# Performance work log

Hardware: AMD Instinct MI355X
Metric: run time of the kernel (lower is better)

The kernel has to match this reference:

```python
import jax, jax.numpy as jnp
import numpy as np

EPS = 1e-5
NUM_HEADS = 8
MASK_FILL = -50000.0


def set_norm(X, fmask):
    # Masked "set" layer-norm: mean/var over ALL valid (row, feature) entries
    # of each set jointly. fmask: [B, S, 1] float (1 = valid row).
    D = X.shape[-1]
    cnt = fmask.sum(axis=(1, 2), keepdims=True) * D
    mean = (X * fmask).sum(axis=(1, 2), keepdims=True) / cnt
    var = (((X - mean) ** 2) * fmask).sum(axis=(1, 2), keepdims=True) / cnt
    return (X - mean) / jnp.sqrt(var + EPS) * fmask


def setup_inputs() -> dict:
    key = jax.random.key(0)
    ks = jax.random.split(key, 9)
    B, S, D = 8, 1024, 512
    Q = jax.random.normal(ks[0], (B, S, D), dtype=jnp.float32)
    Q = Q.at[:, 3 * S // 4:, :].set(0.0)
    scale = 0.02
    params = {
        'Wq': jax.random.normal(ks[1], (D, D), jnp.float32) * scale,
        'bq': jnp.zeros((D,), jnp.float32),
        'Wk': jax.random.normal(ks[2], (D, D), jnp.float32) * scale,
        'bk': jnp.zeros((D,), jnp.float32),
        'Wv': jax.random.normal(ks[3], (D, D), jnp.float32) * scale,
        'bv': jnp.zeros((D,), jnp.float32),
        'Wo': jax.random.normal(ks[4], (D, D), jnp.float32) * scale,
        'bo': jnp.zeros((D,), jnp.float32),
    }
    return {'Q': Q, **params}


def reference(Q, Wq, bq, Wk, bk, Wv, bv, Wo, bo):
    B, S, D = Q.shape
    H = NUM_HEADS
    hd = D // H

    # row mask: row is valid if any feature is nonzero
    row_valid = jnp.any(Q != 0, axis=-1, keepdims=True)      # [B, S, 1] bool
    fmask = row_valid.astype(Q.dtype)                        # [B, S, 1]

    # pre-norms (self-attention: K = V = Q)
    Qn = set_norm(Q, fmask)
    Kn = Qn

    # projections, re-masked
    Qp = (Qn @ Wq + bq) * fmask
    Kp = (Kn @ Wk + bk) * fmask
    Vp = (Kn @ Wv + bv) * fmask

    def to_heads(X):  # [B, S, D] -> [B, H, S, hd]
        return X.reshape(B, S, H, hd).transpose(0, 2, 1, 3)

    q, k, v = to_heads(Qp), to_heads(Kp), to_heads(Vp)

    # attn_mask: True = masked-out pair (invalid row in Q or K)
    invalid = ~(row_valid & row_valid.transpose(0, 2, 1))    # [B, S, S]
    invalid = invalid[:, None, :, :]                         # [B, 1, S, S]

    scale = 1.0 / np.sqrt(hd).astype(np.float32)
    scores = jnp.einsum('bhqd,bhkd->bhqk', q, k) * scale
    scores = scores + jnp.where(invalid, MASK_FILL, 0.0)
    # additive fill + post-softmax multiplicative mask (nonstandard pattern)
    w = jax.nn.softmax(scores, axis=-1) * (~invalid).astype(scores.dtype)

    attn = jnp.einsum('bhqk,bhkd->bhqd', w, v)               # [B, H, S, hd]
    attn = attn.transpose(0, 2, 1, 3).reshape(B, S, D)

    attn_out = attn + Q                                      # residual with raw input
    normed = set_norm(attn_out, fmask)                       # normVO (V mask == Q mask)
    out = attn_out + jax.nn.relu(normed @ Wo + bo)           # dropout p=0 -> identity
    return out, w
```

## Files before the change

### kernel.cpp

```cpp
#include <hip/hip_runtime.h>
#include <math.h>

#define BB 8
#define SS 1024
#define DD 512
#define HH 8
#define NROWS (BB*SS)
#define EPSV 1e-5f
#define SCALE_V 0.125f

#define I_SUM1 0
#define I_SS1  8
#define I_CNT  16
#define I_MEAN1 24
#define I_INV1 32
#define I_SUM2 40
#define I_SS2  48
#define I_MEAN2 56
#define I_INV2 64
#define I_TMASK 96
#define I_KBITS 224

typedef __bf16 bf16x8 __attribute__((ext_vector_type(8)));
typedef __bf16 bf16x4 __attribute__((ext_vector_type(4)));
typedef float f32x4 __attribute__((ext_vector_type(4)));

#define MFMA16(a,b,c) __builtin_amdgcn_mfma_f32_16x16x32_bf16(a,b,c,0,0,0)

#define LDSTRIDE 40
#define ASTR 72

__global__ __launch_bounds__(128) void stats1_k(const float* __restrict__ Q,
                                                float* __restrict__ fmask,
                                                float* __restrict__ stats) {
    int row = blockIdx.x;
    int b = row >> 10;
    int t = threadIdx.x;
    float4 v = *(const float4*)(Q + ((size_t)row << 9) + (t << 2));
    float s  = v.x + v.y + v.z + v.w;
    float ss = v.x*v.x + v.y*v.y + v.z*v.z + v.w*v.w;
    int nz = (v.x != 0.f) || (v.y != 0.f) || (v.z != 0.f) || (v.w != 0.f);
    __shared__ float rs[128], rss[128];
    __shared__ int rnz[128];
    rs[t] = s; rss[t] = ss; rnz[t] = nz;
    __syncthreads();
    for (int off = 64; off > 0; off >>= 1) {
        if (t < off) { rs[t] += rs[t+off]; rss[t] += rss[t+off]; rnz[t] |= rnz[t+off]; }
        __syncthreads();
    }
    if (t == 0) {
        float f = rnz[0] ? 1.f : 0.f;
        fmask[row] = f;
        if (f != 0.f) {
            atomicAdd(&stats[I_SUM1 + b], rs[0]);
            atomicAdd(&stats[I_SS1 + b], rss[0]);
            atomicAdd(&stats[I_CNT + b], 1.f);
        }
    }
}

__global__ __launch_bounds__(128) void finalize_k(float* __restrict__ stats,
                                                  const float* __restrict__ fmask,
                                                  int osum, int oss, int ocnt,
                                                  int omean, int oinv, int dotile) {
    int t = threadIdx.x;
    if (t < BB) {
        float cntD = stats[ocnt + t] * 512.f;
        float mean = stats[osum + t] / cntD;
        float var  = stats[oss + t] / cntD - mean * mean;
        stats[omean + t] = mean;
        stats[oinv + t]  = rsqrtf(var + EPSV);
    }
    if (dotile) {
        int* ip = (int*)stats;
        const float* fr = fmask + (t << 6);
        int any = 0;
        for (int i = 0; i < 64; i += 4) {
            float4 v = *(const float4*)(fr + i);
            any |= (v.x != 0.f) | (v.y != 0.f) | (v.z != 0.f) | (v.w != 0.f);
        }
        ip[I_TMASK + t] = any;
        __syncthreads();
        if (t < BB) {
            int bits = 0;
            #pragma unroll
            for (int i = 0; i < 16; ++i)
                bits |= (ip[I_TMASK + (t << 4) + i] ? 1 : 0) << i;
            ip[I_KBITS + t] = bits;
        }
    }
}

__global__ __launch_bounds__(256) void tw_k(const float* __restrict__ Wq,
                                            const float* __restrict__ Wk,
                                            const float* __restrict__ Wv,
                                            const float* __restrict__ Wo,
                                            __bf16* __restrict__ Wt) {
    int z = blockIdx.z;
    const float* W = (z == 0) ? Wq : (z == 1) ? Wk : (z == 2) ? Wv : Wo;
    __bf16* dst = Wt + ((size_t)z << 18);
    __shared__ float tile[64][65];
    int t = threadIdx.x;
    int k0 = blockIdx.y << 6, n0 = blockIdx.x << 6;
    int r = t >> 4, c = (t & 15) << 2;
    #pragma unroll
    for (int i = 0; i < 4; ++i) {
        float4 v = *(const float4*)(W + (size_t)(k0 + r + i*16) * 512 + n0 + c);
        tile[r + i*16][c+0] = v.x; tile[r + i*16][c+1] = v.y;
        tile[r + i*16][c+2] = v.z; tile[r + i*16][c+3] = v.w;
    }
    __syncthreads();
    #pragma unroll
    for (int i = 0; i < 4; ++i) {
        int n = r + i*16;
        bf16x4 o;
        o[0] = (__bf16)tile[c+0][n]; o[1] = (__bf16)tile[c+1][n];
        o[2] = (__bf16)tile[c+2][n]; o[3] = (__bf16)tile[c+3][n];
        *(bf16x4*)(dst + (size_t)(n0 + n) * 512 + k0 + c) = o;
    }
}

__global__ __launch_bounds__(256) void projqkv_k(
    const float* __restrict__ Q, const float* __restrict__ stats,
    const float* __restrict__ fmask, const __bf16* __restrict__ Wt,
    const float* __restrict__ bq, const float* __restrict__ bk,
    const float* __restrict__ bv,
    __bf16* __restrict__ Qp, __bf16* __restrict__ Kp, __bf16* __restrict__ Vt)
{
    __shared__ __align__(16) __bf16 smem[64 * LDSTRIDE * 4];
    int t = threadIdx.x;
    int m0 = blockIdx.y << 6, n0 = blockIdx.x << 6;
    int b = m0 >> 10, s0 = m0 & 1023, h = n0 >> 6;
    int bh = (b << 3) + h;
    const int* ip = (const int*)stats;
    if (!ip[I_TMASK + (m0 >> 6)]) {
        int m = t >> 2, ch = (t & 3) << 4;
        bf16x8 z = {};
        *(bf16x8*)(Qp + ((size_t)(m0 + m) << 9) + n0 + ch)     = z;
        *(bf16x8*)(Qp + ((size_t)(m0 + m) << 9) + n0 + ch + 8) = z;
        *(bf16x8*)(Kp + ((size_t)(m0 + m) << 9) + n0 + ch)     = z;
        *(bf16x8*)(Kp + ((size_t)(m0 + m) << 9) + n0 + ch + 8) = z;
        *(bf16x8*)(Vt + ((size_t)bh << 16) + ((size_t)m << 10) + s0 + ch)     = z;
        *(bf16x8*)(Vt + ((size_t)bh << 16) + ((size_t)m << 10) + s0 + ch + 8) = z;
        return;
    }
    __bf16* As = smem;
    int srow = t >> 2, skp = (t & 3) << 3;
    int arow = m0 + srow;
    float fi   = fmask[arow] * stats[I_INV1 + b];
    float mean = stats[I_MEAN1 + b];
    int wave = t >> 6, lane = t & 63, quad = lane >> 4, l16 = lane & 15;
    int aoff  = (wave * 16 + l16) * LDSTRIDE + quad * 8;
    int boff0 = l16 * LDSTRIDE + quad * 8;
    f32x4 acc[3][4] = {};
    const float*  Arow = Q + ((size_t)arow << 9);
    const __bf16* Brow = Wt + ((size_t)(n0 + srow) << 9);
    float4 a0 = *(const float4*)(Arow + skp);
    float4 a1 = *(const float4*)(Arow + skp + 4);
    bf16x8 w0 = *(const bf16x8*)(Brow + skp);
    bf16x8 w1 = *(const bf16x8*)(Brow + (1 << 18) + skp);
    bf16x8 w2 = *(const bf16x8*)(Brow + (2 << 18) + skp);
    for (int k0 = 0; k0 < 512; k0 += 32) {
        bf16x8 av;
        av[0] = (__bf16)((a0.x - mean) * fi); av[1] = (__bf16)((a0.y - mean) * fi);
        av[2] = (__bf16)((a0.z - mean) * fi); av[3] = (__bf16)((a0.w - mean) * fi);
        av[4] = (__bf16)((a1.x - mean) * fi); av[5] = (__bf16)((a1.y - mean) * fi);
        av[6] = (__bf16)((a1.z - mean) * fi); av[7] = (__bf16)((a1.w - mean) * fi);
        *(bf16x8*)&As[srow * LDSTRIDE + skp] = av;
        *(bf16x8*)&smem[64*LDSTRIDE*1 + srow * LDSTRIDE + skp] = w0;
        *(bf16x8*)&smem[64*LDSTRIDE*2 + srow * LDSTRIDE + skp] = w1;
        *(bf16x8*)&smem[64*LDSTRIDE*3 + srow * LDSTRIDE + skp] = w2;
        __syncthreads();
        if (k0 < 480) {
            a0 = *(const float4*)(Arow + k0 + 32 + skp);
            a1 = *(const float4*)(Arow + k0 + 36 + skp);
            w0 = *(const bf16x8*)(Brow + k0 + 32 + skp);
            w1 = *(const bf16x8*)(Brow + (1 << 18) + k0 + 32 + skp);
            w2 = *(const bf16x8*)(Brow + (2 << 18) + k0 + 32 + skp);
        }
        bf16x8 af = *(const bf16x8*)&As[aoff];
        #pragma unroll
        for (int nt = 0; nt < 4; ++nt) {
            int bo = boff0 + nt * (16 * LDSTRIDE);
            acc[0][nt] = MFMA16(af, *(const bf16x8*)&smem[64*LDSTRIDE*1 + bo], acc[0][nt]);
            acc[1][nt] = MFMA16(af, *(const bf16x8*)&smem[64*LDSTRIDE*2 + bo], acc[1][nt]);
            acc[2][nt] = MFMA16(af, *(const bf16x8*)&smem[64*LDSTRIDE*3 + bo], acc[2][nt]);
        }
        __syncthreads();
    }
    float fmr[4];
    #pragma unroll
    for (int reg = 0; reg < 4; ++reg) fmr[reg] = fmask[m0 + wave*16 + quad*4 + reg];
    __bf16* Cs = smem;
    #pragma unroll
    for (int z = 0; z < 2; ++z) {
        const float* bias = z ? bk : bq;
        __bf16* C = z ? Kp : Qp;
        #pragma unroll
        for (int nt = 0; nt < 4; ++nt) {
            float bn = bias[n0 + nt * 16 + l16];
            #pragma unroll
            for (int reg = 0; reg < 4; ++reg) {
                int m = wave * 16 + quad * 4 + reg;
                Cs[m * 70 + nt * 16 + l16] = (__bf16)((acc[z][nt][reg] + bn) * fmr[reg]);
            }
        }
        __syncthreads();
        int m = t >> 2, ch = (t & 3) << 4;
        bf16x8 o0 = *(const bf16x8*)&Cs[m * 70 + ch];
        bf16x8 o1 = *(const bf16x8*)&Cs[m * 70 + ch + 8];
        *(bf16x8*)(C + ((size_t)(m0 + m) << 9) + n0 + ch)     = o0;
        *(bf16x8*)(C + ((size_t)(m0 + m) << 9) + n0 + ch + 8) = o1;
        __syncthreads();
    }
    #pragma unroll
    for (int nt = 0; nt < 4; ++nt) {
        int d = nt * 16 + l16;
        float bn = bv[n0 + d];
        #pragma unroll
        for (int reg = 0; reg < 4; ++reg) {
            int sl = wave * 16 + quad * 4 + reg;
            Cs[d * 70 + sl] = (__bf16)((acc[2][nt][reg] + bn) * fmr[reg]);
        }
    }
    __syncthreads();
    {
        int d = t >> 2, seg = (t & 3) << 4;
        bf16x8 o0 = *(const bf16x8*)&Cs[d * 70 + seg];
        bf16x8 o1 = *(const bf16x8*)&Cs[d * 70 + seg + 8];
        *(bf16x8*)(Vt + ((size_t)bh << 16) + ((size_t)d << 10) + s0 + seg)     = o0;
        *(bf16x8*)(Vt + ((size_t)bh << 16) + ((size_t)d << 10) + s0 + seg + 8) = o1;
    }
}

__global__ __launch_bounds__(256) void attn_k(
    const __bf16* __restrict__ Qp, const __bf16* __restrict__ Kp,
    const __bf16* __restrict__ Vt,
    const float* __restrict__ fmask, const float* __restrict__ Q,
    float* __restrict__ stats, float* __restrict__ w, float* __restrict__ attn)
{
    int bh = blockIdx.y, b = bh >> 3, h = bh & 7;
    int q0 = blockIdx.x << 6;
    int t = threadIdx.x;
    const int* ip = (const int*)stats;
    int kb = ip[I_KBITS + b];
    int fb = b << 10;
    size_t wqbase = ((size_t)bh << 20) + ((size_t)q0 << 10);
    if (!((kb >> (q0 >> 6)) & 1)) {
        int q = t >> 2, ch = (t & 3) << 4;
        float4 z4 = {0.f, 0.f, 0.f, 0.f};
        float* wp0 = w + wqbase + ((size_t)q << 10) + ch;
        #pragma unroll
        for (int kc0 = 0; kc0 < 1024; kc0 += 64) {
            *(float4*)(wp0 + kc0)      = z4;
            *(float4*)(wp0 + kc0 + 4)  = z4;
            *(float4*)(wp0 + kc0 + 8)  = z4;
            *(float4*)(wp0 + kc0 + 12) = z4;
        }
        size_t base = ((size_t)(fb + q0 + q) << 9) + (h << 6) + ch;
        #pragma unroll
        for (int i = 0; i < 4; ++i)
            *(float4*)(attn + base + i*4) = *(const float4*)(Q + base + i*4);
        return;
    }
    __shared__ __align__(16) __bf16 Ks[64 * ASTR];
    __shared__ __align__(16) __bf16 Vs[64 * ASTR];
    __shared__ __align__(16) __bf16 Ws[64 * ASTR];
    __shared__ float red[8];
    int wave = t >> 6, lane = t & 63, quad = lane >> 4, l16 = lane & 15;
    int sr = t >> 3, sc = (t & 7) << 3;
    const __bf16* Qr = Qp + ((size_t)(fb + q0 + wave*16 + l16) << 9) + (h << 6) + (quad << 3);
    bf16x8 qa0 = *(const bf16x8*)(Qr);
    bf16x8 qa1 = *(const bf16x8*)(Qr + 32);
    int aoff = (wave * 16 + l16) * ASTR + (quad << 3);

    float rsum[4] = {0.f, 0.f, 0.f, 0.f};
    bf16x8 kr0, kr1;
    bool curok = kb & 1;
    if (curok) {
        kr0 = *(const bf16x8*)(Kp + ((size_t)(fb + sr) << 9) + (h << 6) + sc);
        kr1 = *(const bf16x8*)(Kp + ((size_t)(fb + 32 + sr) << 9) + (h << 6) + sc);
    }
    for (int kc = 0; kc < 16; ++kc) {
        bool nextok = (kc < 15) && ((kb >> (kc + 1)) & 1);
        int nbase = fb + ((kc + 1) << 6);
        if (curok) {
            *(bf16x8*)&Ks[sr * ASTR + sc] = kr0;
            *(bf16x8*)&Ks[(32 + sr) * ASTR + sc] = kr1;
            __syncthreads();
            if (nextok) {
                kr0 = *(const bf16x8*)(Kp + ((size_t)(nbase + sr) << 9) + (h << 6) + sc);
                kr1 = *(const bf16x8*)(Kp + ((size_t)(nbase + 32 + sr) << 9) + (h << 6) + sc);
            }
            int kc0 = kc << 6;
            #pragma unroll
            for (int nt = 0; nt < 4; ++nt) {
                int boff = (nt * 16 + l16) * ASTR + (quad << 3);
                f32x4 s = {};
                s = MFMA16(qa0, *(const bf16x8*)&Ks[boff], s);
                s = MFMA16(qa1, *(const bf16x8*)&Ks[boff + 32], s);
                float fk = fmask[fb + kc0 + nt * 16 + l16];
                #pragma unroll
                for (int r = 0; r < 4; ++r)
                    rsum[r] += (fk != 0.f) ? __expf(s[r] * SCALE_V) : 0.f;
            }
            __syncthreads();
        } else if (nextok) {
            kr0 = *(const bf16x8*)(Kp + ((size_t)(nbase + sr) << 9) + (h << 6) + sc);
            kr1 = *(const bf16x8*)(Kp + ((size_t)(nbase + 32 + sr) << 9) + (h << 6) + sc);
        }
        curok = nextok;
    }
    float inv[4];
    #pragma unroll
    for (int r = 0; r < 4; ++r) {
        float v = rsum[r];
        v += __shfl_xor(v, 1); v += __shfl_xor(v, 2);
        v += __shfl_xor(v, 4); v += __shfl_xor(v, 8);
        float fq = fmask[fb + q0 + wave * 16 + quad * 4 + r];
        inv[r] = (fq != 0.f && v > 0.f) ? 1.f / v : 0.f;
    }

    f32x4 accO[4] = {};
    bf16x8 vr0, vr1;
    curok = kb & 1;
    if (curok) {
        kr0 = *(const bf16x8*)(Kp + ((size_t)(fb + sr) << 9) + (h << 6) + sc);
        kr1 = *(const bf16x8*)(Kp + ((size_t)(fb + 32 + sr) << 9) + (h << 6) + sc);
        vr0 = *(const bf16x8*)(Vt + ((size_t)bh << 16) + ((size_t)sr << 10) + sc);
        vr1 = *(const bf16x8*)(Vt + ((size_t)bh << 16) + ((size_t)(32 + sr) << 10) + sc);
    }
    for (int kc = 0; kc < 16; ++kc) {
        int kc0 = kc << 6;
        bool nextok = (kc < 15) && ((kb >> (kc + 1)) & 1);
        int nk0 = kc0 + 64;
        if (curok) {
            *(bf16x8*)&Ks[sr * ASTR + sc] = kr0;
            *(bf16x8*)&Ks[(32 + sr) * ASTR + sc] = kr1;
            *(bf16x8*)&Vs[sr * ASTR + sc] = vr0;
            *(bf16x8*)&Vs[(32 + sr) * ASTR + sc] = vr1;
            __syncthreads();
            if (nextok) {
                kr0 = *(const bf16x8*)(Kp + ((size_t)(fb + nk0 + sr) << 9) + (h << 6) + sc);
                kr1 = *(const bf16x8*)(Kp + ((size_t)(fb + nk0 + 32 + sr) << 9) + (h << 6) + sc);
                vr0 = *(const bf16x8*)(Vt + ((size_t)bh << 16) + ((size_t)sr << 10) + nk0 + sc);
                vr1 = *(const bf16x8*)(Vt + ((size_t)bh << 16) + ((size_t)(32 + sr) << 10) + nk0 + sc);
            }
            #pragma unroll
            for (int nt = 0; nt < 4; ++nt) {
                int boff = (nt * 16 + l16) * ASTR + (quad << 3);
                f32x4 s = {};
                s = MFMA16(qa0, *(const bf16x8*)&Ks[boff], s);
                s = MFMA16(qa1, *(const bf16x8*)&Ks[boff + 32], s);
                float fk = fmask[fb + kc0 + nt * 16 + l16];
                #pragma unroll
                for (int r = 0; r < 4; ++r) {
                    float p = (fk != 0.f) ? __expf(s[r] * SCALE_V) * inv[r] : 0.f;
                    Ws[(wave * 16 + quad * 4 + r) * ASTR + nt * 16 + l16] = (__bf16)p;
                }
            }
            __syncthreads();
            bf16x8 pa0 = *(const bf16x8*)&Ws[aoff];
            bf16x8 pa1 = *(const bf16x8*)&Ws[aoff + 32];
            #pragma unroll
            for (int nt = 0; nt < 4; ++nt) {
                int boff = (nt * 16 + l16) * ASTR + (quad << 3);
                accO[nt] = MFMA16(pa0, *(const bf16x8*)&Vs[boff], accO[nt]);
                accO[nt] = MFMA16(pa1, *(const bf16x8*)&Vs[boff + 32], accO[nt]);
            }
            {
                int q = t >> 2, ch = (t & 3) << 4;
                bf16x8 w0 = *(const bf16x8*)&Ws[q * ASTR + ch];
                bf16x8 w1 = *(const bf16x8*)&Ws[q * ASTR + ch + 8];
                float4 f0, f1, f2, f3;
                f0.x = (float)w0[0]; f0.y = (float)w0[1]; f0.z = (float)w0[2]; f0.w = (float)w0[3];
                f1.x = (float)w0[4]; f1.y = (float)w0[5]; f1.z = (float)w0[6]; f1.w = (float)w0[7];
                f2.x = (float)w1[0]; f2.y = (float)w1[1]; f2.z = (float)w1[2]; f2.w = (float)w1[3];
                f3.x = (float)w1[4]; f3.y = (float)w1[5]; f3.z = (float)w1[6]; f3.w = (float)w1[7];
                float* wp = w + wqbase + ((size_t)q << 10) + kc0 + ch;
                *(float4*)(wp)      = f0;
                *(float4*)(wp + 4)  = f1;
                *(float4*)(wp + 8)  = f2;
                *(float4*)(wp + 12) = f3;
            }
            __syncthreads();
        } else {
            int q = t >> 2, ch = (t & 3) << 4;
            float4 z4 = {0.f, 0.f, 0.f, 0.f};
            float* wp = w + wqbase + ((size_t)q << 10) + kc0 + ch;
            *(float4*)(wp)      = z4;
            *(float4*)(wp + 4)  = z4;
            *(float4*)(wp + 8)  = z4;
            *(float4*)(wp + 12) = z4;
            if (nextok) {
                kr0 = *(const bf16x8*)(Kp + ((size_t)(fb + nk0 + sr) << 9) + (h << 6) + sc);
                kr1 = *(const bf16x8*)(Kp + ((size_t)(fb + nk0 + 32 + sr) << 9) + (h << 6) + sc);
                vr0 = *(const bf16x8*)(Vt + ((size_t)bh << 16) + ((size_t)sr << 10) + nk0 + sc);
                vr1 = *(const bf16x8*)(Vt + ((size_t)bh << 16) + ((size_t)(32 + sr) << 10) + nk0 + sc);
            }
        }
        curok = nextok;
    }
    float s1 = 0.f, s2 = 0.f;
    #pragma unroll
    for (int nt = 0; nt < 4; ++nt) {
        int d = nt * 16 + l16;
        #pragma unroll
        for (int r = 0; r < 4; ++r) {
            int q = q0 + wave * 16 + quad * 4 + r;
            size_t off = ((size_t)(fb + q) << 9) + (h << 6) + d;
            float v = accO[nt][r] + Q[off];
            attn[off] = v;
            s1 += v; s2 += v * v;
        }
    }
    #pragma unroll
    for (int o = 32; o > 0; o >>= 1) {
        s1 += __shfl_xor(s1, o);
        s2 += __shfl_xor(s2, o);
    }
    if (lane == 0) { red[wave * 2] = s1; red[wave * 2 + 1] = s2; }
    __syncthreads();
    if (t == 0) {
        atomicAdd(&stats[I_SUM2 + b], red[0] + red[2] + red[4] + red[6]);
        atomicAdd(&stats[I_SS2 + b], red[1] + red[3] + red[5] + red[7]);
    }
}

__global__ __launch_bounds__(256) void final_gemm(
    const float* __restrict__ attn, const float* __restrict__ stats,
    const float* __restrict__ fmask, const __bf16* __restrict__ Wot,
    const float* __restrict__ bo, float* __restrict__ out)
{
    int t = threadIdx.x;
    int m0 = blockIdx.y << 6, n0 = blockIdx.x << 6;
    const int* ip = (const int*)stats;
    if (!ip[I_TMASK + (m0 >> 6)]) {
        int m = t >> 2, c = (t & 3) << 4;
        size_t base = ((size_t)(m0 + m) << 9) + n0 + c;
        #pragma unroll
        for (int i = 0; i < 4; ++i) {
            float4 a = *(const float4*)(attn + base + i * 4);
            float4 bb = *(const float4*)(bo + n0 + c + i * 4);
            float4 o;
            o.x = a.x + fmaxf(bb.x, 0.f); o.y = a.y + fmaxf(bb.y, 0.f);
            o.z = a.z + fmaxf(bb.z, 0.f); o.w = a.w + fmaxf(bb.w, 0.f);
            *(float4*)(out + base + i * 4) = o;
        }
        return;
    }
    __shared__ __align__(16) __bf16 smem[64 * LDSTRIDE * 2];
    __bf16* As = smem;
    __bf16* Bs = smem + 64 * LDSTRIDE;
    int srow = t >> 2, skp = (t & 3) << 3;
    int arow = m0 + srow, ab = arow >> 10;
    float fi   = fmask[arow] * stats[I_INV2 + ab];
    float mean = stats[I_MEAN2 + ab];
    int wave = t >> 6, lane = t & 63, quad = lane >> 4, l16 = lane & 15;
    int aoff  = (wave * 16 + l16) * LDSTRIDE + quad * 8;
    int boff0 = l16 * LDSTRIDE + quad * 8;
    f32x4 acc[4] = {};
    const float*  Arow = attn + ((size_t)arow << 9);
    const __bf16* Brow = Wot + ((size_t)(n0 + srow) << 9);
    float4 a0 = *(const float4*)(Arow + skp);
    float4 a1 = *(const float4*)(Arow + skp + 4);
    bf16x8 bw = *(const bf16x8*)(Brow + skp);
    for (int k0 = 0; k0 < 512; k0 += 32) {
        bf16x8 av;
        av[0] = (__bf16)((a0.x - mean) * fi); av[1] = (__bf16)((a0.y - mean) * fi);
        av[2] = (__bf16)((a0.z - mean) * fi); av[3] = (__bf16)((a0.w - mean) * fi);
        av[4] = (__bf16)((a1.x - mean) * fi); av[5] = (__bf16)((a1.y - mean) * fi);
        av[6] = (__bf16)((a1.z - mean) * fi); av[7] = (__bf16)((a1.w - mean) * fi);
        *(bf16x8*)&As[srow * LDSTRIDE + skp] = av;
        *(bf16x8*)&Bs[srow * LDSTRIDE + skp] = bw;
        __syncthreads();
        if (k0 < 480) {
            a0 = *(const float4*)(Arow + k0 + 32 + skp);
            a1 = *(const float4*)(Arow + k0 + 36 + skp);
            bw = *(const bf16x8*)(Brow + k0 + 32 + skp);
        }
        bf16x8 af = *(const bf16x8*)&As[aoff];
        #pragma unroll
        for (int nt = 0; nt < 4; ++nt)
            acc[nt] = MFMA16(af, *(const bf16x8*)&Bs[boff0 + nt * (16 * LDSTRIDE)], acc[nt]);
        __syncthreads();
    }
    #pragma unroll
    for (int nt = 0; nt < 4; ++nt) {
        int n = n0 + nt * 16 + l16;
        float bn = bo[n];
        #pragma unroll
        for (int reg = 0; reg < 4; ++reg) {
            int m = m0 + wave * 16 + quad * 4 + reg;
            size_t off = ((size_t)m << 9) + n;
            out[off] = attn[off] + fmaxf(acc[nt][reg] + bn, 0.f);
        }
    }
}

extern "C" void kernel_launch(void* const* d_in, const int* in_sizes, int n_in,
                              void* d_out, int out_size, void* d_ws, size_t ws_size,
                              hipStream_t stream) {
    const float* Q  = (const float*)d_in[0];
    const float* Wq = (const float*)d_in[1];
    const float* bq = (const float*)d_in[2];
    const float* Wk = (const float*)d_in[3];
    const float* bk = (const float*)d_in[4];
    const float* Wv = (const float*)d_in[5];
    const float* bv = (const float*)d_in[6];
    const float* Wo = (const float*)d_in[7];
    const float* bo = (const float*)d_in[8];
    float* out = (float*)d_out;
    float* w   = out + (size_t)BB * SS * DD;

    char* ws = (char*)d_ws;
    float* stats  = (float*)ws;
    float* fmask  = (float*)(ws + 4096);
    __bf16* Wt = (__bf16*)(ws + 4096 + 32768);
    __bf16* Qp = Wt + ((size_t)4 << 18);
    __bf16* Kp = Qp + ((size_t)NROWS * DD);
    __bf16* Vt = Kp + ((size_t)NROWS * DD);
    float* attn = (float*)(Vt + ((size_t)NROWS * DD));

    (void)hipMemsetAsync(stats, 0, 4096, stream);
    stats1_k<<<NROWS, 128, 0, stream>>>(Q, fmask, stats);
    finalize_k<<<1, 128, 0, stream>>>(stats, fmask, I_SUM1, I_SS1, I_CNT, I_MEAN1, I_INV1, 1);
    tw_k<<<dim3(8, 8, 4), 256, 0, stream>>>(Wq, Wk, Wv, Wo, Wt);
    projqkv_k<<<dim3(8, 128), 256, 0, stream>>>(Q, stats, fmask, Wt,
                                                bq, bk, bv, Qp, Kp, Vt);
    attn_k<<<dim3(16, 64), 256, 0, stream>>>(Qp, Kp, Vt, fmask, Q, stats, w, attn);
    finalize_k<<<1, 128, 0, stream>>>(stats, fmask, I_SUM2, I_SS2, I_CNT, I_MEAN2, I_INV2, 0);
    final_gemm<<<dim3(8, 128), 256, 0, stream>>>(attn, stats, fmask,
                                                 Wt + ((size_t)3 << 18), bo, out);
}
```

Baseline: 589.0 us.

## Single-pass attention caching unnormalized probabilities in LDS with split-K waves

Replaces the two-pass attention (one pass for row sums, one to recompute scores, apply PV and write w) with a single pass. Unnormalized bf16 probabilities for the whole 64x1024 tile are kept in a 128 KB swizzled LDS buffer, and normalization is applied at the end when w is written and when the output is scaled. Blocks now use 512 threads, split into 4 query waves times 2 key-half waves, with a cross-wave reduction of the partial PV accumulators. This removes the recomputation of QK^T and exp and the second reload of K. The cost is heavy LDS usage, which likely limits occupancy to one block per CU, plus an extra bf16 rounding of the unnormalized P before scaling.

Result: slower. 613.1 us (+4.1%).

```diff
diff --git a/kernel.cpp b/kernel.cpp
--- a/kernel.cpp
+++ b/kernel.cpp
@@ -29,6 +29,7 @@
 
 #define LDSTRIDE 40
 #define ASTR 72
+#define PSWZ(row, col) ((((row) << 10) + (col)) ^ (((row) & 7) << 3))
 
 __global__ __launch_bounds__(128) void stats1_k(const float* __restrict__ Q,
                                                 float* __restrict__ fmask,
@@ -233,7 +234,7 @@
     }
 }
 
-__global__ __launch_bounds__(256) void attn_k(
+__global__ __launch_bounds__(512) void attn_k(
     const __bf16* __restrict__ Qp, const __bf16* __restrict__ Kp,
     const __bf16* __restrict__ Vt,
     const float* __restrict__ fmask, const float* __restrict__ Q,
@@ -247,183 +248,162 @@
     int fb = b << 10;
     size_t wqbase = ((size_t)bh << 20) + ((size_t)q0 << 10);
     if (!((kb >> (q0 >> 6)) & 1)) {
-        int q = t >> 2, ch = (t & 3) << 4;
+        int row = t >> 3, coff = (t & 7) << 4;
         float4 z4 = {0.f, 0.f, 0.f, 0.f};
-        float* wp0 = w + wqbase + ((size_t)q << 10) + ch;
-        #pragma unroll
-        for (int kc0 = 0; kc0 < 1024; kc0 += 64) {
-            *(float4*)(wp0 + kc0)      = z4;
-            *(float4*)(wp0 + kc0 + 4)  = z4;
-            *(float4*)(wp0 + kc0 + 8)  = z4;
-            *(float4*)(wp0 + kc0 + 12) = z4;
-        }
-        size_t base = ((size_t)(fb + q0 + q) << 9) + (h << 6) + ch;
-        #pragma unroll
-        for (int i = 0; i < 4; ++i)
-            *(float4*)(attn + base + i*4) = *(const float4*)(Q + base + i*4);
+        float* wp0 = w + wqbase + ((size_t)row << 10) + coff;
+        #pragma unroll
+        for (int j = 0; j < 8; ++j) {
+            float* p = wp0 + (j << 7);
+            *(float4*)(p)      = z4;
+            *(float4*)(p + 4)  = z4;
+            *(float4*)(p + 8)  = z4;
+            *(float4*)(p + 12) = z4;
+        }
+        size_t base = ((size_t)(fb + q0 + row) << 9) + (h << 6) + ((t & 7) << 3);
+        *(float4*)(attn + base)     = *(const float4*)(Q + base);
+        *(float4*)(attn + base + 4) = *(const float4*)(Q + base + 4);
         return;
     }
-    __shared__ __align__(16) __bf16 Ks[64 * ASTR];
-    __shared__ __align__(16) __bf16 Vs[64 * ASTR];
-    __shared__ __align__(16) __bf16 Ws[64 * ASTR];
-    __shared__ float red[8];
+    __shared__ __align__(16) __bf16 P[65536];
+    __shared__ __align__(16) __bf16 KV[2 * 64 * ASTR];
+    __shared__ float red2[128];
+    __shared__ float invld[64];
+    __shared__ float redf[8];
+    __bf16* Ks = KV;
+    __bf16* Vs = KV + 64 * ASTR;
     int wave = t >> 6, lane = t & 63, quad = lane >> 4, l16 = lane & 15;
+    int wq = wave & 3, wk = wave >> 2;
+    int kbase = wk << 5;
     int sr = t >> 3, sc = (t & 7) << 3;
-    const __bf16* Qr = Qp + ((size_t)(fb + q0 + wave*16 + l16) << 9) + (h << 6) + (quad << 3);
+    const __bf16* Qr = Qp + ((size_t)(fb + q0 + (wq << 4) + l16) << 9) + (h << 6) + (quad << 3);
     bf16x8 qa0 = *(const bf16x8*)(Qr);
     bf16x8 qa1 = *(const bf16x8*)(Qr + 32);
-    int aoff = (wave * 16 + l16) * ASTR + (quad << 3);
-
     float rsum[4] = {0.f, 0.f, 0.f, 0.f};
-    bf16x8 kr0, kr1;
+    f32x4 accO[4] = {};
+    bf16x8 kr, vr;
     bool curok = kb & 1;
     if (curok) {
-        kr0 = *(const bf16x8*)(Kp + ((size_t)(fb + sr) << 9) + (h << 6) + sc);
-        kr1 = *(const bf16x8*)(Kp + ((size_t)(fb + 32 + sr) << 9) + (h << 6) + sc);
+        kr = *(const bf16x8*)(Kp + ((size_t)(fb + sr) << 9) + (h << 6) + sc);
+        vr = *(const bf16x8*)(Vt + ((size_t)bh << 16) + ((size_t)sr << 10) + sc);
     }
     for (int kc = 0; kc < 16; ++kc) {
         bool nextok = (kc < 15) && ((kb >> (kc + 1)) & 1);
-        int nbase = fb + ((kc + 1) << 6);
+        int nk0 = (kc + 1) << 6;
         if (curok) {
-            *(bf16x8*)&Ks[sr * ASTR + sc] = kr0;
-            *(bf16x8*)&Ks[(32 + sr) * ASTR + sc] = kr1;
+            __syncthreads();
+            *(bf16x8*)&Ks[sr * ASTR + sc] = kr;
+            *(bf16x8*)&Vs[sr * ASTR + sc] = vr;
             __syncthreads();
             if (nextok) {
-                kr0 = *(const bf16x8*)(Kp + ((size_t)(nbase + sr) << 9) + (h << 6) + sc);
-                kr1 = *(const bf16x8*)(Kp + ((size_t)(nbase + 32 + sr) << 9) + (h << 6) + sc);
+                kr = *(const bf16x8*)(Kp + ((size_t)(fb + nk0 + sr) << 9) + (h << 6) + sc);
+                vr = *(const bf16x8*)(Vt + ((size_t)bh << 16) + ((size_t)sr << 10) + nk0 + sc);
             }
             int kc0 = kc << 6;
             #pragma unroll
-            for (int nt = 0; nt < 4; ++nt) {
-                int boff = (nt * 16 + l16) * ASTR + (quad << 3);
+            for (int nt = 0; nt < 2; ++nt) {
+                int col = kbase + (nt << 4) + l16;
+                int boff = col * ASTR + (quad << 3);
                 f32x4 s = {};
                 s = MFMA16(qa0, *(const bf16x8*)&Ks[boff], s);
                 s = MFMA16(qa1, *(const bf16x8*)&Ks[boff + 32], s);
-                float fk = fmask[fb + kc0 + nt * 16 + l16];
+                float fk = fmask[fb + kc0 + col];
                 #pragma unroll
-                for (int r = 0; r < 4; ++r)
-                    rsum[r] += (fk != 0.f) ? __expf(s[r] * SCALE_V) : 0.f;
+                for (int r = 0; r < 4; ++r) {
+                    float p = (fk != 0.f) ? __expf(s[r] * SCALE_V) : 0.f;
+                    rsum[r] += p;
+                    int prow = (wq << 4) + (quad << 2) + r;
+                    P[PSWZ(prow, kc0 + col)] = (__bf16)p;
+                }
             }
-            __syncthreads();
+            {
+                int prow = (wq << 4) + l16;
+                bf16x8 pa = *(const bf16x8*)&P[PSWZ(prow, kc0 + kbase + (quad << 3))];
+                #pragma unroll
+                for (int nt2 = 0; nt2 < 4; ++nt2) {
+                    int voff = ((nt2 << 4) + l16) * ASTR + kbase + (quad << 3);
+                    accO[nt2] = MFMA16(pa, *(const bf16x8*)&Vs[voff], accO[nt2]);
+                }
+            }
         } else if (nextok) {
-            kr0 = *(const bf16x8*)(Kp + ((size_t)(nbase + sr) << 9) + (h << 6) + sc);
-            kr1 = *(const bf16x8*)(Kp + ((size_t)(nbase + 32 + sr) << 9) + (h << 6) + sc);
+            kr = *(const bf16x8*)(Kp + ((size_t)(fb + nk0 + sr) << 9) + (h << 6) + sc);
+            vr = *(const bf16x8*)(Vt + ((size_t)bh << 16) + ((size_t)sr << 10) + nk0 + sc);
         }
         curok = nextok;
     }
-    float inv[4];
     #pragma unroll
     for (int r = 0; r < 4; ++r) {
         float v = rsum[r];
         v += __shfl_xor(v, 1); v += __shfl_xor(v, 2);
         v += __shfl_xor(v, 4); v += __shfl_xor(v, 8);
-        float fq = fmask[fb + q0 + wave * 16 + quad * 4 + r];
-        inv[r] = (fq != 0.f && v > 0.f) ? 1.f / v : 0.f;
-    }
-
-    f32x4 accO[4] = {};
-    bf16x8 vr0, vr1;
-    curok = kb & 1;
-    if (curok) {
-        kr0 = *(const bf16x8*)(Kp + ((size_t)(fb + sr) << 9) + (h << 6) + sc);
-        kr1 = *(const bf16x8*)(Kp + ((size_t)(fb + 32 + sr) << 9) + (h << 6) + sc);
-        vr0 = *(const bf16x8*)(Vt + ((size_t)bh << 16) + ((size_t)sr << 10) + sc);
-        vr1 = *(const bf16x8*)(Vt + ((size_t)bh << 16) + ((size_t)(32 + sr) << 10) + sc);
-    }
-    for (int kc = 0; kc < 16; ++kc) {
-        int kc0 = kc << 6;
-        bool nextok = (kc < 15) && ((kb >> (kc + 1)) & 1);
-        int nk0 = kc0 + 64;
-        if (curok) {
-            *(bf16x8*)&Ks[sr * ASTR + sc] = kr0;
-            *(bf16x8*)&Ks[(32 + sr) * ASTR + sc] = kr1;
-            *(bf16x8*)&Vs[sr * ASTR + sc] = vr0;
-            *(bf16x8*)&Vs[(32 + sr) * ASTR + sc] = vr1;
-            __syncthreads();
-            if (nextok) {
-                kr0 = *(const bf16x8*)(Kp + ((size_t)(fb + nk0 + sr) << 9) + (h << 6) + sc);
-                kr1 = *(const bf16x8*)(Kp + ((size_t)(fb + nk0 + 32 + sr) << 9) + (h << 6) + sc);
-                vr0 = *(const bf16x8*)(Vt + ((size_t)bh << 16) + ((size_t)sr << 10) + nk0 + sc);
-                vr1 = *(const bf16x8*)(Vt + ((size_t)bh << 16) + ((size_t)(32 + sr) << 10) + nk0 + sc);
+        if (l16 == 0) red2[(((wq << 4) + (quad << 2) + r) << 1) + wk] = v;
+    }
+    __syncthreads();
+    if (t < 64) {
+        float z = red2[t << 1] + red2[(t << 1) + 1];
+        float fq = fmask[fb + q0 + t];
+        invld[t] = (fq != 0.f && z > 0.f) ? 1.f / z : 0.f;
+    }
+    __syncthreads();
+    float* accL = (float*)KV;
+    if (wk == 1) {
+        #pragma unroll
+        for (int nt2 = 0; nt2 < 4; ++nt2)
+            #pragma unroll
+            for (int r = 0; r < 4; ++r)
+                accL[((wq << 4) + (quad << 2) + r) * 65 + (nt2 << 4) + l16] = accO[nt2][r];
+    }
+    {
+        int row = t >> 3, coff = (t & 7) << 4;
+        float iv = invld[row];
+        float* wrow = w + wqbase + ((size_t)row << 10);
+        #pragma unroll
+        for (int j = 0; j < 8; ++j) {
+            int col = coff + (j << 7);
+            float4 f0, f1, f2, f3;
+            if ((kb >> (col >> 6)) & 1) {
+                bf16x8 p0 = *(const bf16x8*)&P[PSWZ(row, col)];
+                bf16x8 p1 = *(const bf16x8*)&P[PSWZ(row, col + 8)];
+                f0.x = (float)p0[0]*iv; f0.y = (float)p0[1]*iv; f0.z = (float)p0[2]*iv; f0.w = (float)p0[3]*iv;
+                f1.x = (float)p0[4]*iv; f1.y = (float)p0[5]*iv; f1.z = (float)p0[6]*iv; f1.w = (float)p0[7]*iv;
+                f2.x = (float)p1[0]*iv; f2.y = (float)p1[1]*iv; f2.z = (float)p1[2]*iv; f2.w = (float)p1[3]*iv;
+                f3.x = (float)p1[4]*iv; f3.y = (float)p1[5]*iv; f3.z = (float)p1[6]*iv; f3.w = (float)p1[7]*iv;
+            } else {
+                f0 = {0.f,0.f,0.f,0.f}; f1 = f0; f2 = f0; f3 = f0;
             }
+            float* p = wrow + col;
+            *(float4*)(p)      = f0;
+            *(float4*)(p + 4)  = f1;
+            *(float4*)(p + 8)  = f2;
+            *(float4*)(p + 12) = f3;
+        }
+    }
+    __syncthreads();
+    if (wk == 0) {
+        float s1 = 0.f, s2 = 0.f;
+        #pragma unroll
+        for (int nt2 = 0; nt2 < 4; ++nt2) {
+            int d = (nt2 << 4) + l16;
             #pragma unroll
-            for (int nt = 0; nt < 4; ++nt) {
-                int boff = (nt * 16 + l16) * ASTR + (quad << 3);
-                f32x4 s = {};
-                s = MFMA16(qa0, *(const bf16x8*)&Ks[boff], s);
-                s = MFMA16(qa1, *(const bf16x8*)&Ks[boff + 32], s);
-                float fk = fmask[fb + kc0 + nt * 16 + l16];
-                #pragma unroll
-                for (int r = 0; r < 4; ++r) {
-                    float p = (fk != 0.f) ? __expf(s[r] * SCALE_V) * inv[r] : 0.f;
-                    Ws[(wave * 16 + quad * 4 + r) * ASTR + nt * 16 + l16] = (__bf16)p;
-                }
+            for (int r = 0; r < 4; ++r) {
+                int row = (wq << 4) + (quad << 2) + r;
+                float o = (accO[nt2][r] + accL[row * 65 + d]) * invld[row];
+                size_t off = ((size_t)(fb + q0 + row) << 9) + (h << 6) + d;
+                float v = o + Q[off];
+                attn[off] = v;
+                s1 += v; s2 += v * v;
             }
-            __syncthreads();
-            bf16x8 pa0 = *(const bf16x8*)&Ws[aoff];
-            bf16x8 pa1 = *(const bf16x8*)&Ws[aoff + 32];
-            #pragma unroll
-            for (int nt = 0; nt < 4; ++nt) {
-                int boff = (nt * 16 + l16) * ASTR + (quad << 3);
-                accO[nt] = MFMA16(pa0, *(const bf16x8*)&Vs[boff], accO[nt]);
-                accO[nt] = MFMA16(pa1, *(const bf16x8*)&Vs[boff + 32], accO[nt]);
-            }
-            {
-                int q = t >> 2, ch = (t & 3) << 4;
-                bf16x8 w0 = *(const bf16x8*)&Ws[q * ASTR + ch];
-                bf16x8 w1 = *(const bf16x8*)&Ws[q * ASTR + ch + 8];
-                float4 f0, f1, f2, f3;
-                f0.x = (float)w0[0]; f0.y = (float)w0[1]; f0.z = (float)w0[2]; f0.w = (float)w0[3];
-                f1.x = (float)w0[4]; f1.y = (float)w0[5]; f1.z = (float)w0[6]; f1.w = (float)w0[7];
-                f2.x = (float)w1[0]; f2.y = (float)w1[1]; f2.z = (float)w1[2]; f2.w = (float)w1[3];
-                f3.x = (float)w1[4]; f3.y = (float)w1[5]; f3.z = (float)w1[6]; f3.w = (float)w1[7];
-                float* wp = w + wqbase + ((size_t)q << 10) + kc0 + ch;
-                *(float4*)(wp)      = f0;
-                *(float4*)(wp + 4)  = f1;
-                *(float4*)(wp + 8)  = f2;
-                *(float4*)(wp + 12) = f3;
-            }
-            __syncthreads();
-        } else {
-            int q = t >> 2, ch = (t & 3) << 4;
-            float4 z4 = {0.f, 0.f, 0.f, 0.f};
-            float* wp = w + wqbase + ((size_t)q << 10) + kc0 + ch;
-            *(float4*)(wp)      = z4;
-            *(float4*)(wp + 4)  = z4;
-            *(float4*)(wp + 8)  = z4;
-            *(float4*)(wp + 12) = z4;
-            if (nextok) {
-                kr0 = *(const bf16x8*)(Kp + ((size_t)(fb + nk0 + sr) << 9) + (h << 6) + sc);
-                kr1 = *(const bf16x8*)(Kp + ((size_t)(fb + nk0 + 32 + sr) << 9) + (h << 6) + sc);
-                vr0 = *(const bf16x8*)(Vt + ((size_t)bh << 16) + ((size_t)sr << 10) + nk0 + sc);
-                vr1 = *(const bf16x8*)(Vt + ((size_t)bh << 16) + ((size_t)(32 + sr) << 10) + nk0 + sc);
-            }
-        }
-        curok = nextok;
-    }
-    float s1 = 0.f, s2 = 0.f;
-    #pragma unroll
-    for (int nt = 0; nt < 4; ++nt) {
-        int d = nt * 16 + l16;
-        #pragma unroll
-        for (int r = 0; r < 4; ++r) {
-            int q = q0 + wave * 16 + quad * 4 + r;
-            size_t off = ((size_t)(fb + q) << 9) + (h << 6) + d;
-            float v = accO[nt][r] + Q[off];
-            attn[off] = v;
-            s1 += v; s2 += v * v;
-        }
-    }
-    #pragma unroll
-    for (int o = 32; o > 0; o >>= 1) {
-        s1 += __shfl_xor(s1, o);
-        s2 += __shfl_xor(s2, o);
-    }
-    if (lane == 0) { red[wave * 2] = s1; red[wave * 2 + 1] = s2; }
+        }
+        #pragma unroll
+        for (int o = 32; o > 0; o >>= 1) {
+            s1 += __shfl_xor(s1, o);
+            s2 += __shfl_xor(s2, o);
+        }
+        if (lane == 0) { redf[wq * 2] = s1; redf[wq * 2 + 1] = s2; }
+    }
     __syncthreads();
     if (t == 0) {
-        atomicAdd(&stats[I_SUM2 + b], red[0] + red[2] + red[4] + red[6]);
-        atomicAdd(&stats[I_SS2 + b], red[1] + red[3] + red[5] + red[7]);
+        atomicAdd(&stats[I_SUM2 + b], redf[0] + redf[2] + redf[4] + redf[6]);
+        atomicAdd(&stats[I_SS2 + b], redf[1] + redf[3] + redf[5] + redf[7]);
     }
 }
 
@@ -528,7 +508,7 @@
     tw_k<<<dim3(8, 8, 4), 256, 0, stream>>>(Wq, Wk, Wv, Wo, Wt);
     projqkv_k<<<dim3(8, 128), 256, 0, stream>>>(Q, stats, fmask, Wt,
                                                 bq, bk, bv, Qp, Kp, Vt);
-    attn_k<<<dim3(16, 64), 256, 0, stream>>>(Qp, Kp, Vt, fmask, Q, stats, w, attn);
+    attn_k<<<dim3(16, 64), 512, 0, stream>>>(Qp, Kp, Vt, fmask, Q, stats, w, attn);
     finalize_k<<<1, 128, 0, stream>>>(stats, fmask, I_SUM2, I_SS2, I_CNT, I_MEAN2, I_INV2, 0);
     final_gemm<<<dim3(8, 128), 256, 0, stream>>>(attn, stats, fmask,
                                                  Wt + ((size_t)3 << 18), bo, out);
```

## Double query tile per attention block and double-buffer K/V shared tiles

Applied to the files above, without the earlier changes.

Each attention block now handles 128 query rows instead of 64, with each wave computing two 16-row groups. The goal is to reuse every K and V tile loaded into shared memory across twice as many queries, halving K/V global traffic per query. K and V shared buffers are ping-ponged so one of the two per-iteration barriers can be dropped. In exchange there are fewer blocks (512 instead of 1024), more registers and shared memory per block, and the skip path for fully masked tiles now only fires when both 64-row halves are invalid.

Measured after the change: 624.6 us. +6.0%, slower.

```diff
diff --git a/kernel.cpp b/kernel.cpp
--- a/kernel.cpp
+++ b/kernel.cpp
@@ -240,89 +240,107 @@
     float* __restrict__ stats, float* __restrict__ w, float* __restrict__ attn)
 {
     int bh = blockIdx.y, b = bh >> 3, h = bh & 7;
-    int q0 = blockIdx.x << 6;
+    int q0 = blockIdx.x << 7;
     int t = threadIdx.x;
     const int* ip = (const int*)stats;
     int kb = ip[I_KBITS + b];
     int fb = b << 10;
     size_t wqbase = ((size_t)bh << 20) + ((size_t)q0 << 10);
-    if (!((kb >> (q0 >> 6)) & 1)) {
-        int q = t >> 2, ch = (t & 3) << 4;
+    int qt0 = q0 >> 6;
+    if (!(((kb >> qt0) & 1) || ((kb >> (qt0 + 1)) & 1))) {
+        int rr = t >> 2, ch = (t & 3) << 4;
         float4 z4 = {0.f, 0.f, 0.f, 0.f};
-        float* wp0 = w + wqbase + ((size_t)q << 10) + ch;
-        #pragma unroll
-        for (int kc0 = 0; kc0 < 1024; kc0 += 64) {
-            *(float4*)(wp0 + kc0)      = z4;
-            *(float4*)(wp0 + kc0 + 4)  = z4;
-            *(float4*)(wp0 + kc0 + 8)  = z4;
-            *(float4*)(wp0 + kc0 + 12) = z4;
-        }
-        size_t base = ((size_t)(fb + q0 + q) << 9) + (h << 6) + ch;
-        #pragma unroll
-        for (int i = 0; i < 4; ++i)
-            *(float4*)(attn + base + i*4) = *(const float4*)(Q + base + i*4);
+        #pragma unroll
+        for (int rb = 0; rb < 128; rb += 64) {
+            float* wp0 = w + wqbase + ((size_t)(rb + rr) << 10) + ch;
+            #pragma unroll
+            for (int kc0 = 0; kc0 < 1024; kc0 += 64) {
+                *(float4*)(wp0 + kc0)      = z4;
+                *(float4*)(wp0 + kc0 + 4)  = z4;
+                *(float4*)(wp0 + kc0 + 8)  = z4;
+                *(float4*)(wp0 + kc0 + 12) = z4;
+            }
+            size_t base = ((size_t)(fb + q0 + rb + rr) << 9) + (h << 6) + ch;
+            #pragma unroll
+            for (int i = 0; i < 4; ++i)
+                *(float4*)(attn + base + i*4) = *(const float4*)(Q + base + i*4);
+        }
         return;
     }
-    __shared__ __align__(16) __bf16 Ks[64 * ASTR];
-    __shared__ __align__(16) __bf16 Vs[64 * ASTR];
-    __shared__ __align__(16) __bf16 Ws[64 * ASTR];
+    __shared__ __align__(16) __bf16 KsA[64 * ASTR];
+    __shared__ __align__(16) __bf16 KsB[64 * ASTR];
+    __shared__ __align__(16) __bf16 VsA[64 * ASTR];
+    __shared__ __align__(16) __bf16 VsB[64 * ASTR];
+    __shared__ __align__(16) __bf16 Ws[128 * ASTR];
     __shared__ float red[8];
     int wave = t >> 6, lane = t & 63, quad = lane >> 4, l16 = lane & 15;
     int sr = t >> 3, sc = (t & 7) << 3;
-    const __bf16* Qr = Qp + ((size_t)(fb + q0 + wave*16 + l16) << 9) + (h << 6) + (quad << 3);
-    bf16x8 qa0 = *(const bf16x8*)(Qr);
-    bf16x8 qa1 = *(const bf16x8*)(Qr + 32);
-    int aoff = (wave * 16 + l16) * ASTR + (quad << 3);
-
-    float rsum[4] = {0.f, 0.f, 0.f, 0.f};
-    bf16x8 kr0, kr1;
+    bf16x8 qa[2][2];
+    #pragma unroll
+    for (int g = 0; g < 2; ++g) {
+        const __bf16* Qr = Qp + ((size_t)(fb + q0 + wave*32 + g*16 + l16) << 9) + (h << 6) + (quad << 3);
+        qa[g][0] = *(const bf16x8*)(Qr);
+        qa[g][1] = *(const bf16x8*)(Qr + 32);
+    }
+
+    float rsum[2][4] = {};
+    bf16x8 kr0, kr1, vr0, vr1;
     bool curok = kb & 1;
     if (curok) {
         kr0 = *(const bf16x8*)(Kp + ((size_t)(fb + sr) << 9) + (h << 6) + sc);
         kr1 = *(const bf16x8*)(Kp + ((size_t)(fb + 32 + sr) << 9) + (h << 6) + sc);
     }
+    int ai = 0;
     for (int kc = 0; kc < 16; ++kc) {
         bool nextok = (kc < 15) && ((kb >> (kc + 1)) & 1);
-        int nbase = fb + ((kc + 1) << 6);
+        int nb = fb + ((kc + 1) << 6);
         if (curok) {
-            *(bf16x8*)&Ks[sr * ASTR + sc] = kr0;
-            *(bf16x8*)&Ks[(32 + sr) * ASTR + sc] = kr1;
+            __bf16* Kd = (ai & 1) ? KsB : KsA;
+            *(bf16x8*)&Kd[sr * ASTR + sc] = kr0;
+            *(bf16x8*)&Kd[(32 + sr) * ASTR + sc] = kr1;
             __syncthreads();
             if (nextok) {
-                kr0 = *(const bf16x8*)(Kp + ((size_t)(nbase + sr) << 9) + (h << 6) + sc);
-                kr1 = *(const bf16x8*)(Kp + ((size_t)(nbase + 32 + sr) << 9) + (h << 6) + sc);
+                kr0 = *(const bf16x8*)(Kp + ((size_t)(nb + sr) << 9) + (h << 6) + sc);
+                kr1 = *(const bf16x8*)(Kp + ((size_t)(nb + 32 + sr) << 9) + (h << 6) + sc);
             }
             int kc0 = kc << 6;
             #pragma unroll
             for (int nt = 0; nt < 4; ++nt) {
                 int boff = (nt * 16 + l16) * ASTR + (quad << 3);
-                f32x4 s = {};
-                s = MFMA16(qa0, *(const bf16x8*)&Ks[boff], s);
-                s = MFMA16(qa1, *(const bf16x8*)&Ks[boff + 32], s);
+                bf16x8 kf0 = *(const bf16x8*)&Kd[boff];
+                bf16x8 kf1 = *(const bf16x8*)&Kd[boff + 32];
                 float fk = fmask[fb + kc0 + nt * 16 + l16];
                 #pragma unroll
-                for (int r = 0; r < 4; ++r)
-                    rsum[r] += (fk != 0.f) ? __expf(s[r] * SCALE_V) : 0.f;
-            }
-            __syncthreads();
+                for (int g = 0; g < 2; ++g) {
+                    f32x4 s = {};
+                    s = MFMA16(qa[g][0], kf0, s);
+                    s = MFMA16(qa[g][1], kf1, s);
+                    #pragma unroll
+                    for (int r = 0; r < 4; ++r)
+                        rsum[g][r] += (fk != 0.f) ? __expf(s[r] * SCALE_V) : 0.f;
+                }
+            }
+            ++ai;
         } else if (nextok) {
-            kr0 = *(const bf16x8*)(Kp + ((size_t)(nbase + sr) << 9) + (h << 6) + sc);
-            kr1 = *(const bf16x8*)(Kp + ((size_t)(nbase + 32 + sr) << 9) + (h << 6) + sc);
+            kr0 = *(const bf16x8*)(Kp + ((size_t)(nb + sr) << 9) + (h << 6) + sc);
+            kr1 = *(const bf16x8*)(Kp + ((size_t)(nb + 32 + sr) << 9) + (h << 6) + sc);
         }
         curok = nextok;
     }
-    float inv[4];
-    #pragma unroll
-    for (int r = 0; r < 4; ++r) {
-        float v = rsum[r];
-        v += __shfl_xor(v, 1); v += __shfl_xor(v, 2);
-        v += __shfl_xor(v, 4); v += __shfl_xor(v, 8);
-        float fq = fmask[fb + q0 + wave * 16 + quad * 4 + r];
-        inv[r] = (fq != 0.f && v > 0.f) ? 1.f / v : 0.f;
-    }
-
-    f32x4 accO[4] = {};
-    bf16x8 vr0, vr1;
+    float inv[2][4];
+    #pragma unroll
+    for (int g = 0; g < 2; ++g)
+        #pragma unroll
+        for (int r = 0; r < 4; ++r) {
+            float v = rsum[g][r];
+            v += __shfl_xor(v, 1); v += __shfl_xor(v, 2);
+            v += __shfl_xor(v, 4); v += __shfl_xor(v, 8);
+            float fq = fmask[fb + q0 + wave*32 + g*16 + quad*4 + r];
+            inv[g][r] = (fq != 0.f && v > 0.f) ? 1.f / v : 0.f;
+        }
+    __syncthreads();
+
+    f32x4 accO[2][4] = {};
     curok = kb & 1;
     if (curok) {
         kr0 = *(const bf16x8*)(Kp + ((size_t)(fb + sr) << 9) + (h << 6) + sc);
@@ -330,15 +348,18 @@
         vr0 = *(const bf16x8*)(Vt + ((size_t)bh << 16) + ((size_t)sr << 10) + sc);
         vr1 = *(const bf16x8*)(Vt + ((size_t)bh << 16) + ((size_t)(32 + sr) << 10) + sc);
     }
+    ai = 0;
     for (int kc = 0; kc < 16; ++kc) {
         int kc0 = kc << 6;
         bool nextok = (kc < 15) && ((kb >> (kc + 1)) & 1);
         int nk0 = kc0 + 64;
         if (curok) {
-            *(bf16x8*)&Ks[sr * ASTR + sc] = kr0;
-            *(bf16x8*)&Ks[(32 + sr) * ASTR + sc] = kr1;
-            *(bf16x8*)&Vs[sr * ASTR + sc] = vr0;
-            *(bf16x8*)&Vs[(32 + sr) * ASTR + sc] = vr1;
+            __bf16* Kd = (ai & 1) ? KsB : KsA;
+            __bf16* Vd = (ai & 1) ? VsB : VsA;
+            *(bf16x8*)&Kd[sr * ASTR + sc] = kr0;
+            *(bf16x8*)&Kd[(32 + sr) * ASTR + sc] = kr1;
+            *(bf16x8*)&Vd[sr * ASTR + sc] = vr0;
+            *(bf16x8*)&Vd[(32 + sr) * ASTR + sc] = vr1;
             __syncthreads();
             if (nextok) {
                 kr0 = *(const bf16x8*)(Kp + ((size_t)(fb + nk0 + sr) << 9) + (h << 6) + sc);
@@ -349,49 +370,59 @@
             #pragma unroll
             for (int nt = 0; nt < 4; ++nt) {
                 int boff = (nt * 16 + l16) * ASTR + (quad << 3);
-                f32x4 s = {};
-                s = MFMA16(qa0, *(const bf16x8*)&Ks[boff], s);
-                s = MFMA16(qa1, *(const bf16x8*)&Ks[boff + 32], s);
+                bf16x8 kf0 = *(const bf16x8*)&Kd[boff];
+                bf16x8 kf1 = *(const bf16x8*)&Kd[boff + 32];
                 float fk = fmask[fb + kc0 + nt * 16 + l16];
                 #pragma unroll
-                for (int r = 0; r < 4; ++r) {
-                    float p = (fk != 0.f) ? __expf(s[r] * SCALE_V) * inv[r] : 0.f;
-                    Ws[(wave * 16 + quad * 4 + r) * ASTR + nt * 16 + l16] = (__bf16)p;
+                for (int g = 0; g < 2; ++g) {
+                    f32x4 s = {};
+                    s = MFMA16(qa[g][0], kf0, s);
+                    s = MFMA16(qa[g][1], kf1, s);
+                    #pragma unroll
+                    for (int r = 0; r < 4; ++r) {
+                        float p = (fk != 0.f) ? __expf(s[r] * SCALE_V) * inv[g][r] : 0.f;
+                        Ws[(wave*32 + g*16 + quad*4 + r) * ASTR + nt*16 + l16] = (__bf16)p;
+                    }
                 }
             }
-            __syncthreads();
-            bf16x8 pa0 = *(const bf16x8*)&Ws[aoff];
-            bf16x8 pa1 = *(const bf16x8*)&Ws[aoff + 32];
-            #pragma unroll
-            for (int nt = 0; nt < 4; ++nt) {
-                int boff = (nt * 16 + l16) * ASTR + (quad << 3);
-                accO[nt] = MFMA16(pa0, *(const bf16x8*)&Vs[boff], accO[nt]);
-                accO[nt] = MFMA16(pa1, *(const bf16x8*)&Vs[boff + 32], accO[nt]);
+            #pragma unroll
+            for (int g = 0; g < 2; ++g) {
+                int prow = wave*32 + g*16 + l16;
+                bf16x8 pa0 = *(const bf16x8*)&Ws[prow * ASTR + (quad << 3)];
+                bf16x8 pa1 = *(const bf16x8*)&Ws[prow * ASTR + 32 + (quad << 3)];
+                #pragma unroll
+                for (int nt2 = 0; nt2 < 4; ++nt2) {
+                    int voff = (nt2 * 16 + l16) * ASTR + (quad << 3);
+                    accO[g][nt2] = MFMA16(pa0, *(const bf16x8*)&Vd[voff], accO[g][nt2]);
+                    accO[g][nt2] = MFMA16(pa1, *(const bf16x8*)&Vd[voff + 32], accO[g][nt2]);
+                }
             }
             {
-                int q = t >> 2, ch = (t & 3) << 4;
-                bf16x8 w0 = *(const bf16x8*)&Ws[q * ASTR + ch];
-                bf16x8 w1 = *(const bf16x8*)&Ws[q * ASTR + ch + 8];
-                float4 f0, f1, f2, f3;
-                f0.x = (float)w0[0]; f0.y = (float)w0[1]; f0.z = (float)w0[2]; f0.w = (float)w0[3];
-                f1.x = (float)w0[4]; f1.y = (float)w0[5]; f1.z = (float)w0[6]; f1.w = (float)w0[7];
-                f2.x = (float)w1[0]; f2.y = (float)w1[1]; f2.z = (float)w1[2]; f2.w = (float)w1[3];
-                f3.x = (float)w1[4]; f3.y = (float)w1[5]; f3.z = (float)w1[6]; f3.w = (float)w1[7];
-                float* wp = w + wqbase + ((size_t)q << 10) + kc0 + ch;
-                *(float4*)(wp)      = f0;
-                *(float4*)(wp + 4)  = f1;
-                *(float4*)(wp + 8)  = f2;
-                *(float4*)(wp + 12) = f3;
-            }
-            __syncthreads();
+                int row = t >> 1, ch = (t & 1) << 5;
+                float* wp = w + wqbase + ((size_t)row << 10) + kc0 + ch;
+                #pragma unroll
+                for (int jj = 0; jj < 2; ++jj) {
+                    bf16x8 p0 = *(const bf16x8*)&Ws[row * ASTR + ch + jj*16];
+                    bf16x8 p1 = *(const bf16x8*)&Ws[row * ASTR + ch + jj*16 + 8];
+                    float4 f0, f1, f2, f3;
+                    f0.x = (float)p0[0]; f0.y = (float)p0[1]; f0.z = (float)p0[2]; f0.w = (float)p0[3];
+                    f1.x = (float)p0[4]; f1.y = (float)p0[5]; f1.z = (float)p0[6]; f1.w = (float)p0[7];
+                    f2.x = (float)p1[0]; f2.y = (float)p1[1]; f2.z = (float)p1[2]; f2.w = (float)p1[3];
+                    f3.x = (float)p1[4]; f3.y = (float)p1[5]; f3.z = (float)p1[6]; f3.w = (float)p1[7];
+                    *(float4*)(wp + jj*16)      = f0;
+                    *(float4*)(wp + jj*16 + 4)  = f1;
+                    *(float4*)(wp + jj*16 + 8)  = f2;
+                    *(float4*)(wp + jj*16 + 12) = f3;
+                }
+            }
+            ++ai;
         } else {
-            int q = t >> 2, ch = (t & 3) << 4;
+            int row = t >> 1, ch = (t & 1) << 5;
             float4 z4 = {0.f, 0.f, 0.f, 0.f};
-            float* wp = w + wqbase + ((size_t)q << 10) + kc0 + ch;
-            *(float4*)(wp)      = z4;
-            *(float4*)(wp + 4)  = z4;
-            *(float4*)(wp + 8)  = z4;
-            *(float4*)(wp + 12) = z4;
+            float* wp = w + wqbase + ((size_t)row << 10) + kc0 + ch;
+            #pragma unroll
+            for (int jj = 0; jj < 8; ++jj)
+                *(float4*)(wp + (jj << 2)) = z4;
             if (nextok) {
                 kr0 = *(const bf16x8*)(Kp + ((size_t)(fb + nk0 + sr) << 9) + (h << 6) + sc);
                 kr1 = *(const bf16x8*)(Kp + ((size_t)(fb + nk0 + 32 + sr) << 9) + (h << 6) + sc);
@@ -403,17 +434,19 @@
     }
     float s1 = 0.f, s2 = 0.f;
     #pragma unroll
-    for (int nt = 0; nt < 4; ++nt) {
-        int d = nt * 16 + l16;
-        #pragma unroll
-        for (int r = 0; r < 4; ++r) {
-            int q = q0 + wave * 16 + quad * 4 + r;
-            size_t off = ((size_t)(fb + q) << 9) + (h << 6) + d;
-            float v = accO[nt][r] + Q[off];
-            attn[off] = v;
-            s1 += v; s2 += v * v;
-        }
-    }
+    for (int g = 0; g < 2; ++g)
+        #pragma unroll
+        for (int nt2 = 0; nt2 < 4; ++nt2) {
+            int d = nt2 * 16 + l16;
+            #pragma unroll
+            for (int r = 0; r < 4; ++r) {
+                int row = q0 + wave*32 + g*16 + quad*4 + r;
+                size_t off = ((size_t)(fb + row) << 9) + (h << 6) + d;
+                float v = accO[g][nt2][r] + Q[off];
+                attn[off] = v;
+                s1 += v; s2 += v * v;
+            }
+        }
     #pragma unroll
     for (int o = 32; o > 0; o >>= 1) {
         s1 += __shfl_xor(s1, o);
@@ -528,7 +561,7 @@
     tw_k<<<dim3(8, 8, 4), 256, 0, stream>>>(Wq, Wk, Wv, Wo, Wt);
     projqkv_k<<<dim3(8, 128), 256, 0, stream>>>(Q, stats, fmask, Wt,
                                                 bq, bk, bv, Qp, Kp, Vt);
-    attn_k<<<dim3(16, 64), 256, 0, stream>>>(Qp, Kp, Vt, fmask, Q, stats, w, attn);
+    attn_k<<<dim3(8, 64), 256, 0, stream>>>(Qp, Kp, Vt, fmask, Q, stats, w, attn);
     finalize_k<<<1, 128, 0, stream>>>(stats, fmask, I_SUM2, I_SS2, I_CNT, I_MEAN2, I_INV2, 0);
     final_gemm<<<dim3(8, 128), 256, 0, stream>>>(attn, stats, fmask,
                                                  Wt + ((size_t)3 << 18), bo, out);
```
